# Optimization experiments

Hardware: AMD Instinct MI355X
Metric: run time of the kernel (lower is better)

The kernel has to match this reference:

```python
import jax, jax.numpy as jnp
import numpy as np

B, IN_UNITS, IN_CH, NUM_UNITS, UNIT_SIZE = 32, 16, 2048, 16, 64
NUM_ITERS = 2


def setup_inputs() -> dict:
    key = jax.random.key(0)
    k1, k2 = jax.random.split(key)
    x = jax.random.normal(k1, (B, IN_UNITS, IN_CH), dtype=jnp.float32)
    W = jax.random.normal(k2, (1, IN_CH, NUM_UNITS, UNIT_SIZE, IN_UNITS), dtype=jnp.float32)
    return {"x": x, "W": W}


def squash(s):
    # torch code sums squared magnitude over dim=2 (the num_units axis) with keepdim
    mag_sq = jnp.sum(s * s, axis=2, keepdims=True)
    mag = jnp.sqrt(mag_sq)
    return mag_sq / (1.0 + mag_sq) * (s / mag)


def reference(x, W):
    # x: (B, in_units, in_channels) -> (B, in_channels, in_units)
    xt = jnp.swapaxes(x, 1, 2)
    # u_hat[b,i,j,k] = sum_u W[0,i,j,k,u] * xt[b,i,u]  -> (B, IC, NU, US)
    u_hat = jnp.einsum('ijku,biu->bijk', W[0], xt)
    b_ij = jnp.zeros((1, IN_CH, NUM_UNITS, 1), dtype=x.dtype)
    v_j = None
    for _ in range(NUM_ITERS):
        # softmax over a singleton trailing dim -> all ones (faithful to source)
        c_ij = jax.nn.softmax(b_ij, axis=-1)  # (1, IC, NU, 1), broadcasts over batch
        s_j = jnp.sum(c_ij[None, ..., 0][0][None].squeeze(0) * 0 + c_ij * u_hat, axis=1, keepdims=True) if False else jnp.sum(c_ij * u_hat, axis=1, keepdims=True)  # (B,1,NU,US)
        v_j = squash(s_j)  # (B,1,NU,US)
        # agreement: <u_hat, v_j> over unit_size, broadcast v_j over in_channels
        u_vj1 = jnp.einsum('bijk,bljk->bij', u_hat, v_j)  # (B, IC, NU)
        u_vj1 = jnp.mean(u_vj1, axis=0, keepdims=True)[..., None]  # (1, IC, NU, 1)
        b_ij = b_ij + u_vj1
    return v_j[:, 0, :, :]  # (B, num_units, unit_size)
```

## Files before the change

kernel.cpp:

```cpp
#include <hip/hip_runtime.h>
#include <hip/hip_bf16.h>


#define B_SZ   32
#define IC     2048
#define NJ     16
#define NK     64
#define SOUT   (B_SZ*NJ*NK)
#define KSTEPS 1024
#define KSPLIT 64
#define SPW    (KSTEPS/KSPLIT)
#define BATCH  4

typedef float v4f __attribute__((ext_vector_type(4)));
typedef short v8s __attribute__((ext_vector_type(8)));
typedef unsigned int v4u __attribute__((ext_vector_type(4)));

static __device__ inline ushort f2bf(float f) {
    uint32_t u = __float_as_uint(f);
    u += 0x7FFFu + ((u >> 16) & 1u);
    return (ushort)(u >> 16);
}

static __device__ inline uint packbf(float f0, float f1) {
    uint u0 = __float_as_uint(f0) + 0x8000u;
    uint u1 = __float_as_uint(f1) + 0x8000u;
    return __builtin_amdgcn_perm(u1, u0, 0x07060302u);
}

__global__ __launch_bounds__(256)
void caps_xprep(const float* __restrict__ x, ushort* __restrict__ xb) {
    int gid  = blockIdx.x * 256 + threadIdx.x;
    int lane = gid & 63;
    int mt   = (gid >> 6) & 1;
    int step = gid >> 7;
    int q    = lane >> 4;
    int b    = mt * 16 + (lane & 15);
    int i    = 2 * step + (q >> 1);
    int u0   = (q & 1) * 8;

    const float* xp = x + (size_t)b * (16 * IC) + (size_t)u0 * IC + i;
    ushort tmp[8];
    #pragma unroll
    for (int jj = 0; jj < 8; ++jj)
        tmp[jj] = f2bf(xp[(size_t)jj * IC]);
    *(v8s*)(xb + (size_t)gid * 8) = *(const v8s*)tmp;
}

__global__ __launch_bounds__(256)
void caps_mfma(const ushort* __restrict__ xb, const float* __restrict__ W,
               float* __restrict__ part) {
    const int tid   = threadIdx.x;
    const int wv    = tid >> 6;
    const int lane  = tid & 63;
    const int j     = blockIdx.x;
    const int split = blockIdx.y;
    const int n     = lane & 15;
    const int q     = lane >> 4;
    const int step0 = split * SPW;

    v4f acc0 = {0.f, 0.f, 0.f, 0.f};
    v4f acc1 = {0.f, 0.f, 0.f, 0.f};

    const float*  wp = W + (size_t)(2 * step0 + (q >> 1)) * 16384
                         + (size_t)j * 1024 + (size_t)(wv * 16 + n) * 16 + (q & 1) * 8;
    const ushort* xp = xb + (size_t)step0 * 1024 + (size_t)lane * 8;

    #pragma unroll 1
    for (int ss = 0; ss < SPW / BATCH; ++ss) {
        float4 wb0[BATCH], wb1[BATCH];
        v8s    ab0[BATCH], ab1[BATCH];
        #pragma unroll
        for (int t = 0; t < BATCH; ++t) {
            const float*  wpt = wp + (size_t)t * (2 * 16384);
            const ushort* xpt = xp + (size_t)t * 1024;
            wb0[t] = *(const float4*)(wpt);
            wb1[t] = *(const float4*)(wpt + 4);
            ab0[t] = *(const v8s*)(xpt);
            ab1[t] = *(const v8s*)(xpt + 512);
        }
        #pragma unroll
        for (int t = 0; t < BATCH; ++t) {
            v4u pk;
            pk.x = packbf(wb0[t].x, wb0[t].y); pk.y = packbf(wb0[t].z, wb0[t].w);
            pk.z = packbf(wb1[t].x, wb1[t].y); pk.w = packbf(wb1[t].z, wb1[t].w);
            v8s bb = *(v8s*)&pk;
            acc0 = __builtin_amdgcn_mfma_f32_16x16x32_bf16(ab0[t], bb, acc0, 0, 0, 0);
            acc1 = __builtin_amdgcn_mfma_f32_16x16x32_bf16(ab1[t], bb, acc1, 0, 0, 0);
        }
        wp += (size_t)BATCH * 2 * 16384;
        xp += (size_t)BATCH * 1024;
    }

    float* pp = part + (size_t)split * SOUT + (size_t)j * NK + wv * 16 + n;
    #pragma unroll
    for (int r = 0; r < 4; ++r) {
        int m = q * 4 + r;
        pp[(size_t)m * 1024]        = acc0[r];
        pp[(size_t)(m + 16) * 1024] = acc1[r];
    }
}

__global__ __launch_bounds__(256)
void caps_finish(const float* __restrict__ part, float* __restrict__ out) {
    __shared__ float ls[256];
    const int blk = blockIdx.x;
    const int b   = blk >> 2;
    const int k0  = (blk & 3) * 16;
    const int t   = threadIdx.x;
    const int jj  = t >> 4;
    const int kc  = t & 15;
    const size_t idx = (size_t)b * 1024 + (size_t)jj * NK + k0 + kc;

    float s = 0.0f;
    #pragma unroll 8
    for (int sp = 0; sp < KSPLIT; ++sp)
        s += part[(size_t)sp * SOUT + idx];
    ls[t] = s;
    __syncthreads();

    float msq = 0.0f;
    #pragma unroll
    for (int j2 = 0; j2 < NJ; ++j2) {
        float v = ls[j2 * 16 + kc];
        msq += v * v;
    }
    float mag = sqrtf(msq);
    out[idx] = s * (mag / (1.0f + msq));
}

extern "C" void kernel_launch(void* const* d_in, const int* in_sizes, int n_in,
                              void* d_out, int out_size, void* d_ws, size_t ws_size,
                              hipStream_t stream) {
    const float* x = (const float*)d_in[0];
    const float* W = (const float*)d_in[1];
    float* out  = (float*)d_out;

    float*  part = (float*)d_ws;
    ushort* xb   = (ushort*)(part + (size_t)KSPLIT * SOUT);

    caps_xprep <<<512,               256, 0, stream>>>(x, xb);
    caps_mfma  <<<dim3(16, KSPLIT),  256, 0, stream>>>(xb, W, part);
    caps_finish<<<128,               256, 0, stream>>>(part, out);
}
```

Measured before the change: 205.6 us.

## Stream W into LDS with double-buffered async global_load_lds and halve K-split

The MFMA kernel now copies W rows straight into a double-buffered LDS area using global_load_lds. The next segment's copy is issued while the current segment is computed, so W loads are fully coalesced and overlap with math. The K-split drops from 64 to 32, giving each block more steps and fewer partial buffers for the finish kernel to reduce. The cost is 64KB of LDS per block, which limits occupancy, plus a barrier per segment and fewer blocks in the grid.

```diff
diff --git a/kernel.cpp b/kernel.cpp
--- a/kernel.cpp
+++ b/kernel.cpp
@@ -8,9 +8,11 @@
 #define NK     64
 #define SOUT   (B_SZ*NJ*NK)
 #define KSTEPS 1024
-#define KSPLIT 64
+#define KSPLIT 32
 #define SPW    (KSTEPS/KSPLIT)
-#define BATCH  4
+#define SEGST  4
+#define NSEG   (SPW/SEGST)
+#define RPS    (2*SEGST)
 
 typedef float v4f __attribute__((ext_vector_type(4)));
 typedef short v8s __attribute__((ext_vector_type(8)));
@@ -50,6 +52,8 @@
 __global__ __launch_bounds__(256)
 void caps_mfma(const ushort* __restrict__ xb, const float* __restrict__ W,
                float* __restrict__ part) {
+    __shared__ float buf[2][RPS * 1024];
+
     const int tid   = threadIdx.x;
     const int wv    = tid >> 6;
     const int lane  = tid & 63;
@@ -57,39 +61,58 @@
     const int split = blockIdx.y;
     const int n     = lane & 15;
     const int q     = lane >> 4;
-    const int step0 = split * SPW;
+    const int i0    = split * (2 * SPW);
+
+    const float*  wjb   = W  + (size_t)j * 1024;
+    const ushort* xbase = xb + (size_t)split * SPW * 1024 + (size_t)lane * 8;
 
     v4f acc0 = {0.f, 0.f, 0.f, 0.f};
     v4f acc1 = {0.f, 0.f, 0.f, 0.f};
 
-    const float*  wp = W + (size_t)(2 * step0 + (q >> 1)) * 16384
-                         + (size_t)j * 1024 + (size_t)(wv * 16 + n) * 16 + (q & 1) * 8;
-    const ushort* xp = xb + (size_t)step0 * 1024 + (size_t)lane * 8;
+    #define STAGE_SEG(seg, bufsel)                                            \
+        do {                                                                  \
+            _Pragma("unroll")                                                 \
+            for (int r = 0; r < RPS; ++r) {                                   \
+                const float* g = wjb +                                        \
+                    (size_t)(i0 + (seg) * RPS + r) * 16384 + tid * 4;         \
+                __builtin_amdgcn_global_load_lds(                             \
+                    (const __attribute__((address_space(1))) void*)g,         \
+                    (__attribute__((address_space(3))) void*)                 \
+                        &buf[bufsel][r * 1024 + wv * 256],                    \
+                    16, 0, 0);                                                \
+            }                                                                 \
+        } while (0)
+
+    STAGE_SEG(0, 0);
+
+    const int fo = (wv * 16 + n) * 16 + (q & 1) * 8;
 
     #pragma unroll 1
-    for (int ss = 0; ss < SPW / BATCH; ++ss) {
-        float4 wb0[BATCH], wb1[BATCH];
-        v8s    ab0[BATCH], ab1[BATCH];
+    for (int sg = 0; sg < NSEG; ++sg) {
+        const int cur = sg & 1;
+        __syncthreads();
+        if (sg + 1 < NSEG) STAGE_SEG(sg + 1, cur ^ 1);
+
+        v8s xa0[SEGST], xa1[SEGST];
         #pragma unroll
-        for (int t = 0; t < BATCH; ++t) {
-            const float*  wpt = wp + (size_t)t * (2 * 16384);
-            const ushort* xpt = xp + (size_t)t * 1024;
-            wb0[t] = *(const float4*)(wpt);
-            wb1[t] = *(const float4*)(wpt + 4);
-            ab0[t] = *(const v8s*)(xpt);
-            ab1[t] = *(const v8s*)(xpt + 512);
+        for (int t = 0; t < SEGST; ++t) {
+            const ushort* xp = xbase + (size_t)(sg * SEGST + t) * 1024;
+            xa0[t] = *(const v8s*)(xp);
+            xa1[t] = *(const v8s*)(xp + 512);
         }
+
         #pragma unroll
-        for (int t = 0; t < BATCH; ++t) {
+        for (int t = 0; t < SEGST; ++t) {
+            const float* bp = &buf[cur][(2 * t + (q >> 1)) * 1024 + fo];
+            float4 w0 = *(const float4*)(bp);
+            float4 w1 = *(const float4*)(bp + 4);
             v4u pk;
-            pk.x = packbf(wb0[t].x, wb0[t].y); pk.y = packbf(wb0[t].z, wb0[t].w);
-            pk.z = packbf(wb1[t].x, wb1[t].y); pk.w = packbf(wb1[t].z, wb1[t].w);
+            pk.x = packbf(w0.x, w0.y); pk.y = packbf(w0.z, w0.w);
+            pk.z = packbf(w1.x, w1.y); pk.w = packbf(w1.z, w1.w);
             v8s bb = *(v8s*)&pk;
-            acc0 = __builtin_amdgcn_mfma_f32_16x16x32_bf16(ab0[t], bb, acc0, 0, 0, 0);
-            acc1 = __builtin_amdgcn_mfma_f32_16x16x32_bf16(ab1[t], bb, acc1, 0, 0, 0);
+            acc0 = __builtin_amdgcn_mfma_f32_16x16x32_bf16(xa0[t], bb, acc0, 0, 0, 0);
+            acc1 = __builtin_amdgcn_mfma_f32_16x16x32_bf16(xa1[t], bb, acc1, 0, 0, 0);
         }
-        wp += (size_t)BATCH * 2 * 16384;
-        xp += (size_t)BATCH * 1024;
     }
 
     float* pp = part + (size_t)split * SOUT + (size_t)j * NK + wv * 16 + n;
```

Result: no change. 208.0 us (+1.2%).
